# Kernel optimization log

Measured on AMD Instinct MI355X. Metric: run time of the kernel, lower is better.

The kernel has to match this reference:

```python
import jax, jax.numpy as jnp
import numpy as np

N_LAYERS = 6
E_DIM = 128
H_DIM = 768
N_HEADS = 12
D_FFN = 3072
SEQ_L = 512
N_WORD = 30000
BATCH = 4
D_HEAD = H_DIM // N_HEADS


def matrix_r(L, d, reverse=False):
    # sinusoidal position matrix, matching torch matrixR
    inv_freq = 1.0 / (10000.0 ** (np.arange(0, d, 2, dtype=np.float32) / d))
    t = np.outer(np.arange(L, dtype=np.float32), inv_freq)
    mat = np.zeros((L, d), dtype=np.float32)
    mat[:, 0::2] = np.sin(t)
    mat[:, 1::2] = np.cos(t)
    if reverse:
        mat = mat[::-1].copy()
    return jnp.asarray(mat)


def _ln(x, g, b, eps=1e-5):
    mu = jnp.mean(x, axis=-1, keepdims=True)
    var = jnp.mean((x - mu) ** 2, axis=-1, keepdims=True)
    return (x - mu) / jnp.sqrt(var + eps) * g + b


def _gelu(x):
    return x * jax.nn.sigmoid(1.702 * x)


def _shift(B):
    # Transformer-XL shift/skew trick: prepend zero column, reshape, drop row, tril
    b, h, L, _ = B.shape
    z = jnp.zeros((b, h, L, 1), B.dtype)
    return jnp.tril(jnp.concatenate([z, B], axis=-1).reshape(b, h, L + 1, L)[:, :, 1:, :])


def _attn_block(x, R, Wq, Wke, Wv, Wkr, cb, pb, Wo_w, Wo_b, g1, b1):
    b, L, H = x.shape
    h, dh = N_HEADS, D_HEAD
    q = (x @ Wq).reshape(b, L, h, dh).transpose(0, 2, 1, 3)   # bhld
    k = (x @ Wke).reshape(b, L, h, dh).transpose(0, 2, 1, 3)
    v = (x @ Wv).reshape(b, L, h, dh).transpose(0, 2, 1, 3)
    Q = (R @ Wkr).reshape(L, h, dh).transpose(1, 0, 2)        # (h, L, dh)
    A_a = jnp.einsum('bhid,bhjd->bhij', q, k)                  # content-content
    Bt = jnp.einsum('bhid,hjd->bhij', q, Q)                    # content-position
    cb_h = cb.reshape(h, dh)
    pb_h = pb.reshape(h, dh)
    A_c = jnp.einsum('hd,bhjd->bhj', cb_h, k)[:, :, None, :]   # global content bias
    D_row = jnp.einsum('hd,hjd->hj', pb_h, Q)                  # global position bias
    D = jnp.broadcast_to(D_row[None, :, None, :], (b, h, L, L))
    A = A_a + _shift(Bt) + A_c + _shift(D)                     # no 1/sqrt(d) scaling in source
    p = jax.nn.softmax(A, axis=-1)
    Oh = jnp.einsum('bhij,bhjd->bhid', p, v)
    O = Oh.transpose(0, 2, 1, 3).reshape(b, L, H)
    return _ln(x + O @ Wo_w + Wo_b, g1, b1)


def setup_inputs() -> dict:
    key = jax.random.key(0)
    ks = jax.random.split(key, 20)
    s = 0.02

    def nrm(k, shape):
        return jax.random.normal(k, shape, jnp.float32) * s

    N, H, F, L = N_LAYERS, H_DIM, D_FFN, SEQ_L
    R0 = matrix_r(L, H, reverse=True)
    inp = {
        'batch': jax.random.randint(ks[0], (BATCH, SEQ_L), 0, N_WORD),
        'seglens': jax.random.randint(ks[1], (BATCH, 2), 0, 200),
        'tok_emb': nrm(ks[2], (N_WORD, E_DIM)),
        'to_hid_w': nrm(ks[3], (E_DIM, H)),
        'to_hid_b': jnp.zeros((H,), jnp.float32),
        'R': jnp.broadcast_to(R0[None], (N, L, H)).copy() if hasattr(jnp.broadcast_to(R0[None], (N, L, H)), 'copy') else jnp.tile(R0[None], (N, 1, 1)),
        'Wq': nrm(ks[4], (N, H, H)),
        'Wke': nrm(ks[5], (N, H, H)),
        'Wv': nrm(ks[6], (N, H, H)),
        'Wkr': nrm(ks[7], (N, H, H)),
        'cb': jnp.ones((N, H), jnp.float32),
        'pb': jnp.ones((N, H), jnp.float32),
        'Wo_w': nrm(ks[8], (N, H, H)),
        'Wo_b': jnp.zeros((N, H), jnp.float32),
        'ln1_g': jnp.ones((N, H), jnp.float32),
        'ln1_b': jnp.zeros((N, H), jnp.float32),
        'ff1_w': nrm(ks[9], (N, H, F)),
        'ff1_b': jnp.zeros((N, F), jnp.float32),
        'ff2_w': nrm(ks[10], (N, F, H)),
        'ff2_b': jnp.zeros((N, H), jnp.float32),
        'ln2_g': jnp.ones((N, H), jnp.float32),
        'ln2_b': jnp.zeros((N, H), jnp.float32),
        'osp_w': nrm(ks[11], (H, 2)),
        'osp_b': jnp.zeros((2,), jnp.float32),
        'mlm_w': nrm(ks[12], (H, H)),
        'mlm_b': jnp.zeros((H,), jnp.float32),
        'mlm_ln_g': jnp.ones((H,), jnp.float32),
        'mlm_ln_b': jnp.zeros((H,), jnp.float32),
        'to_emb_w': nrm(ks[13], (H, E_DIM)),
        'to_emb_b': jnp.zeros((E_DIM,), jnp.float32),
        'out_b': jnp.zeros((N_WORD,), jnp.float32),
    }
    return inp


def reference(batch, seglens, tok_emb, to_hid_w, to_hid_b, R, Wq, Wke, Wv, Wkr, cb, pb,
              Wo_w, Wo_b, ln1_g, ln1_b, ff1_w, ff1_b, ff2_w, ff2_b, ln2_g, ln2_b,
              osp_w, osp_b, mlm_w, mlm_b, mlm_ln_g, mlm_ln_b, to_emb_w, to_emb_b, out_b):
    # seglens is unused by the original forward (mode='pretrain')
    pe = matrix_r(SEQ_L, H_DIM)[None]                      # (1, L, H) absolute positions
    x = tok_emb[batch] @ to_hid_w + to_hid_b + pe          # (B, L, H)
    for i in range(N_LAYERS):
        x = _attn_block(x, R[i], Wq[i], Wke[i], Wv[i], Wkr[i], cb[i], pb[i],
                        Wo_w[i], Wo_b[i], ln1_g[i], ln1_b[i])
        x = _ln(x + _gelu(x @ ff1_w[i] + ff1_b[i]) @ ff2_w[i] + ff2_b[i], ln2_g[i], ln2_b[i])
    C = x[:, 0, :] @ osp_w + osp_b                          # (B, 2) SOP head
    m = _ln(_gelu(x[:, 1:, :] @ mlm_w + mlm_b), mlm_ln_g, mlm_ln_b)
    T = (m @ to_emb_w + to_emb_b) @ tok_emb.T + out_b       # (B, L-1, n_word) tied logits
    return (C, T)
```

## Files before the change

### kernel.cpp

```cpp
#include <hip/hip_runtime.h>
#include <hip/hip_bf16.h>
#include <math.h>

typedef __hip_bfloat16 bf16;
typedef unsigned short ushort_t;
typedef __attribute__((ext_vector_type(8))) short bf16x8;
typedef __attribute__((ext_vector_type(4))) float f32x4;

#define N_LAYERS 6
#define E_DIM 128
#define H_DIM 768
#define N_HEADS 12
#define D_FFN 3072
#define SEQ_L 512
#define N_WORD 30000
#define BATCH 4
#define D_HEAD 64

__device__ __forceinline__ float ldin(const void* p, long i, int fb) {
    return fb ? __bfloat162float(((const bf16*)p)[i]) : ((const float*)p)[i];
}
__device__ __forceinline__ void stout(void* p, long i, float v, int fb) {
    if (fb) ((bf16*)p)[i] = __float2bfloat16(v);
    else    ((float*)p)[i] = v;
}

__global__ void detect_k(const void* g, int* flag)
{
    if (threadIdx.x == 0) {
        const unsigned short* u = (const unsigned short*)g;
        *flag = (u[0] == 0x3F80u) ? 1 : 0;
    }
}

__global__ __launch_bounds__(256)
void embed_k(const int* __restrict__ batch, const void* __restrict__ emb,
             const void* __restrict__ W, const void* __restrict__ bvec,
             float* __restrict__ x, const int* __restrict__ flagp)
{
    int fb = *flagp;
    int tkn = blockIdx.x;
    int l = tkn & 511;
    int idx = batch[tkn];
    __shared__ float e[E_DIM];
    int t = threadIdx.x;
    if (t < E_DIM) e[t] = ldin(emb, (long)idx * E_DIM + t, fb);
    __syncthreads();
    for (int j = t; j < H_DIM; j += 256) {
        float s = 0.f;
        #pragma unroll 8
        for (int k = 0; k < E_DIM; ++k) s += e[k] * ldin(W, (long)k * H_DIM + j, fb);
        s += ldin(bvec, j, fb);
        int m2 = j & ~1;
        float inv = powf(10000.f, -(float)m2 / 768.f);
        float tt = (float)l * inv;
        s += (j & 1) ? cosf(tt) : sinf(tt);
        x[(long)tkn * H_DIM + j] = s;
    }
}

__device__ __forceinline__ void split8(const float* v, uint4& hi, uint4& lo)
{
    unsigned h[4], l[4];
    #pragma unroll
    for (int u = 0; u < 4; ++u) {
        float a = v[2 * u], b = v[2 * u + 1];
        unsigned ba = __float_as_uint(a), bb = __float_as_uint(b);
        unsigned ha = ba & 0xFFFF0000u, hb = bb & 0xFFFF0000u;
        float la = a - __uint_as_float(ha);
        float lb = b - __uint_as_float(hb);
        h[u] = (ha >> 16) | hb;
        l[u] = (__float_as_uint(la) >> 16) | (__float_as_uint(lb) & 0xFFFF0000u);
    }
    hi = make_uint4(h[0], h[1], h[2], h[3]);
    lo = make_uint4(l[0], l[1], l[2], l[3]);
}

template<int BM, int BN, int TPB>
__global__ __launch_bounds__(TPB)
void gemm2(const void* __restrict__ Ap, long aoff0, int lda, long sA1, long sA2,
           const void* __restrict__ Bp, long boff0, int ldb, long sB1, long sB2,
           float* __restrict__ Cp, long coff0, int ldc, long sC1, long sC2,
           int N, int K, int nb2,
           const void* __restrict__ bias, long biasoff, int bstr, int bfp32, int act,
           int amode, int bmode, int bT, int cmode, int flip, int qkv,
           const void* __restrict__ Bp1, const void* __restrict__ Bp2,
           const void* __restrict__ Bp3,
           const void* __restrict__ ApR, long aoffR, float* __restrict__ CpR,
           long cqstride,
           const int* __restrict__ flagp)
{
    constexpr int WAVES = TPB / 64;
    constexpr int WC = (BN >= 128) ? 4 : 2;
    constexpr int WR = WAVES / WC;
    constexpr int FM = (BM / WR) / 16;
    constexpr int FN = (BN / WC) / 16;
    constexpr int AS = BM * 8;
    constexpr int BS = BN * 8;
    constexpr int APT = AS / TPB;
    constexpr int BPT = BS / TPB;
    static_assert(APT >= 1 && BPT >= 1, "tile/threads");

    __shared__ uint4 sAh[AS], sAl[AS], sBh[BS], sBl[BS];

    int fb = *flagp;
    int z = blockIdx.z;
    int z1 = z / nb2, z2 = z - z1 * nb2;
    int I0 = (flip ? blockIdx.x : blockIdx.y) * BM;
    int J0 = (flip ? blockIdx.y : blockIdx.x) * BN;

    const void* A = Ap;
    const void* B = Bp;
    long aoff = aoff0 + z1 * sA1 + z2 * sA2;
    long bofz = boff0 + z1 * sB1 + z2 * sB2;
    float* C = Cp + coff0 + z1 * sC1 + z2 * sC2;
    int am = amode;

    if (qkv) {
        if (z == 3) {
            if (I0 >= 512) return;
            A = ApR; aoff = aoffR; am = 1; C = CpR;
            B = Bp3;
        } else {
            A = Ap; aoff = aoff0;
            B = (z == 0) ? Bp : (z == 1) ? Bp1 : Bp2;
            C = Cp + coff0 + (long)z * cqstride;
        }
        bofz = boff0;
    }

    bool abf = (am == 1) && fb;
    bool bbf = (bmode == 1) && fb;

    int t = threadIdx.x;
    int lane = t & 63;
    int w = t >> 6, wr = w / WC, wc = w % WC;

    f32x4 acc[FM][FN];
    #pragma unroll
    for (int m = 0; m < FM; ++m)
        #pragma unroll
        for (int n = 0; n < FN; ++n)
            #pragma unroll
            for (int q = 0; q < 4; ++q) acc[m][n][q] = 0.f;

    float fA[APT][8]; uint4 uA[APT];
    float fB[BPT][8]; uint4 uB[BPT];
    ushort_t hBv[BPT][8];

    auto FETCH = [&](int k0) {
        #pragma unroll
        for (int p = 0; p < APT; ++p) {
            int s = t + p * TPB;
            int fi = s >> 6, ln = s & 63;
            int ks = fi / (BM / 16), fr = fi - ks * (BM / 16);
            int r = fr * 16 + (ln & 15);
            int kc = ks * 32 + ((ln >> 4) & 3) * 8;
            long g = aoff + (long)(I0 + r) * lda + (k0 + kc);
            if (abf) {
                uA[p] = *(const uint4*)((const ushort_t*)A + g);
            } else {
                *(float4*)&fA[p][0] = *(const float4*)((const float*)A + g);
                *(float4*)&fA[p][4] = *(const float4*)((const float*)A + g + 4);
            }
        }
        #pragma unroll
        for (int p = 0; p < BPT; ++p) {
            int s = t + p * TPB;
            int fi = s >> 6, ln = s & 63;
            int ks = fi / (BN / 16), fc = fi - ks * (BN / 16);
            int col = fc * 16 + (ln & 15);
            int kc = ks * 32 + ((ln >> 4) & 3) * 8;
            int gc = J0 + col;
            if (bT) {
                bool ok = gc < N;
                long g = bofz + (long)gc * ldb + (k0 + kc);
                if (bbf) {
                    uB[p] = ok ? *(const uint4*)((const ushort_t*)B + g)
                               : make_uint4(0, 0, 0, 0);
                } else if (ok) {
                    *(float4*)&fB[p][0] = *(const float4*)((const float*)B + g);
                    *(float4*)&fB[p][4] = *(const float4*)((const float*)B + g + 4);
                } else {
                    #pragma unroll
                    for (int u = 0; u < 8; ++u) fB[p][u] = 0.f;
                }
            } else {
                long g = bofz + (long)(k0 + kc) * ldb + gc;
                if (bbf) {
                    #pragma unroll
                    for (int u = 0; u < 8; ++u)
                        hBv[p][u] = ((const ushort_t*)B)[g + (long)u * ldb];
                } else {
                    #pragma unroll
                    for (int u = 0; u < 8; ++u)
                        fB[p][u] = ((const float*)B)[g + (long)u * ldb];
                }
            }
        }
    };

    auto STORE = [&]() {
        #pragma unroll
        for (int p = 0; p < APT; ++p) {
            int s = t + p * TPB;
            if (abf) {
                sAh[s] = uA[p];
            } else {
                uint4 hi, lo; split8(fA[p], hi, lo);
                sAh[s] = hi; sAl[s] = lo;
            }
        }
        #pragma unroll
        for (int p = 0; p < BPT; ++p) {
            int s = t + p * TPB;
            if (bbf) {
                if (bT) sBh[s] = uB[p];
                else sBh[s] = make_uint4(
                    (unsigned)hBv[p][0] | ((unsigned)hBv[p][1] << 16),
                    (unsigned)hBv[p][2] | ((unsigned)hBv[p][3] << 16),
                    (unsigned)hBv[p][4] | ((unsigned)hBv[p][5] << 16),
                    (unsigned)hBv[p][6] | ((unsigned)hBv[p][7] << 16));
            } else {
                uint4 hi, lo; split8(fB[p], hi, lo);
                sBh[s] = hi; sBl[s] = lo;
            }
        }
    };

    auto COMPUTE = [&]() {
        #pragma unroll
        for (int ks = 0; ks < 2; ++ks) {
            const bf16x8* Ah = (const bf16x8*)sAh + ks * (BM / 16) * 64;
            const bf16x8* Al = (const bf16x8*)sAl + ks * (BM / 16) * 64;
            const bf16x8* Bh = (const bf16x8*)sBh + ks * (BN / 16) * 64;
            const bf16x8* Bl = (const bf16x8*)sBl + ks * (BN / 16) * 64;
            bf16x8 ah[FM], bh[FN];
            #pragma unroll
            for (int m = 0; m < FM; ++m) ah[m] = Ah[(wr * FM + m) * 64 + lane];
            #pragma unroll
            for (int n = 0; n < FN; ++n) bh[n] = Bh[(wc * FN + n) * 64 + lane];
            #pragma unroll
            for (int m = 0; m < FM; ++m)
                #pragma unroll
                for (int n = 0; n < FN; ++n)
                    acc[m][n] = __builtin_amdgcn_mfma_f32_16x16x32_bf16(
                        ah[m], bh[n], acc[m][n], 0, 0, 0);
            if (!abf) {
                bf16x8 al[FM];
                #pragma unroll
                for (int m = 0; m < FM; ++m) al[m] = Al[(wr * FM + m) * 64 + lane];
                #pragma unroll
                for (int m = 0; m < FM; ++m)
                    #pragma unroll
                    for (int n = 0; n < FN; ++n)
                        acc[m][n] = __builtin_amdgcn_mfma_f32_16x16x32_bf16(
                            al[m], bh[n], acc[m][n], 0, 0, 0);
            }
            if (!bbf) {
                bf16x8 bl[FN];
                #pragma unroll
                for (int n = 0; n < FN; ++n) bl[n] = Bl[(wc * FN + n) * 64 + lane];
                #pragma unroll
                for (int m = 0; m < FM; ++m)
                    #pragma unroll
                    for (int n = 0; n < FN; ++n)
                        acc[m][n] = __builtin_amdgcn_mfma_f32_16x16x32_bf16(
                            ah[m], bl[n], acc[m][n], 0, 0, 0);
            }
        }
    };

    FETCH(0);
    for (int k0 = 0; k0 < K; k0 += 64) {
        STORE();
        __syncthreads();
        if (k0 + 64 < K) FETCH(k0 + 64);
        COMPUTE();
        __syncthreads();
    }

    int rl = (lane >> 4) * 4, cl = lane & 15;
    if (cmode == 0) {
        #pragma unroll
        for (int m = 0; m < FM; ++m) {
            #pragma unroll
            for (int n = 0; n < FN; ++n) {
                int col = J0 + wc * (BN / WC) + n * 16 + cl;
                float bv = 0.f;
                if (bias) bv = bfp32 ? ((const float*)bias)[biasoff + (long)z2 * bstr + col]
                                     : ldin(bias, biasoff + (long)z2 * bstr + col, fb);
                #pragma unroll
                for (int j = 0; j < 4; ++j) {
                    int row = I0 + wr * (BM / WR) + m * 16 + rl + j;
                    float v = acc[m][n][j] + bv;
                    if (act == 1) v = v / (1.f + expf(-1.702f * v));
                    C[(long)row * ldc + col] = v;
                }
            }
        }
    } else {
        #pragma unroll
        for (int m = 0; m < FM; ++m) {
            #pragma unroll
            for (int n = 0; n < FN; ++n) {
                int col = J0 + wc * (BN / WC) + n * 16 + cl;
                if (col >= N) continue;
                float bv = ldin(bias, biasoff + col, fb);
                #pragma unroll
                for (int j = 0; j < 4; ++j) {
                    int row = I0 + wr * (BM / WR) + m * 16 + rl + j;
                    int b = row >> 9, l = row & 511;
                    if (l == 0) continue;
                    long ri = (long)b * 511 + (l - 1);
                    stout((void*)C, 8 + ri * (long)N_WORD + col, acc[m][n][j] + bv, fb);
                }
            }
        }
    }
}

__global__ __launch_bounds__(256)
void attn_k(const float* __restrict__ qb, const float* __restrict__ kb,
            const float* __restrict__ vb, const float* __restrict__ BQ,
            const float* __restrict__ kkb, float* __restrict__ out, int bq0)
{
    __shared__ uint4 sQh[512], sQl[512];
    __shared__ uint4 sKh[512], sKl[512];
    __shared__ uint4 sVh[512], sVl[512];
    __shared__ ushort_t sPh[4096], sPl[4096];

    int qt = blockIdx.x;
    int by = blockIdx.y;
    int h  = by % 12;
    int bq = bq0 + by / 12;
    const float* BQh = BQ + (long)by * 262144;
    const float* kkrow = kkb + ((long)(bq * 12 + h)) * 512;
    long qrow0 = (long)bq * 512 + qt * 64;
    long krow0 = (long)bq * 512;

    int t = threadIdx.x;
    int lane = t & 63;
    int w = t >> 6;
    int l4 = (lane >> 4) & 3, l15 = lane & 15;

    #pragma unroll
    for (int p = 0; p < 2; ++p) {
        int s = t + p * 256;
        int fi = s >> 6, ln = s & 63;
        int ks = fi >> 2, fr = fi & 3;
        int r = fr * 16 + (ln & 15);
        int kc = ks * 32 + ((ln >> 4) & 3) * 8;
        const float* g = qb + (qrow0 + r) * 768 + h * 64 + kc;
        float v[8];
        *(float4*)(v)     = *(const float4*)g;
        *(float4*)(v + 4) = *(const float4*)(g + 4);
        uint4 hi, lo; split8(v, hi, lo);
        sQh[s] = hi; sQl[s] = lo;
    }
    __syncthreads();
    bf16x8 qh[2], ql[2];
    #pragma unroll
    for (int ks = 0; ks < 2; ++ks) {
        qh[ks] = ((const bf16x8*)sQh)[(ks * 4 + w) * 64 + lane];
        ql[ks] = ((const bf16x8*)sQl)[(ks * 4 + w) * 64 + lane];
    }

    float mrun[4], lrun[4];
    f32x4 oacc[4];
    #pragma unroll
    for (int j = 0; j < 4; ++j) { mrun[j] = -3e38f; lrun[j] = 0.f; }
    #pragma unroll
    for (int n = 0; n < 4; ++n)
        #pragma unroll
        for (int j = 0; j < 4; ++j) oacc[n][j] = 0.f;

    for (int kt = 0; kt < 8; ++kt) {
        __syncthreads();
        #pragma unroll
        for (int p = 0; p < 2; ++p) {
            int s = t + p * 256;
            int fi = s >> 6, ln = s & 63;
            int ks = fi >> 2, fc = fi & 3;
            int j = fc * 16 + (ln & 15);
            int kc = ks * 32 + ((ln >> 4) & 3) * 8;
            const float* g = kb + (krow0 + kt * 64 + j) * 768 + h * 64 + kc;
            float v[8];
            *(float4*)(v)     = *(const float4*)g;
            *(float4*)(v + 4) = *(const float4*)(g + 4);
            uint4 hi, lo; split8(v, hi, lo);
            sKh[s] = hi; sKl[s] = lo;
        }
        #pragma unroll
        for (int p = 0; p < 2; ++p) {
            int s = t + p * 256;
            int fi = s >> 6, ln = s & 63;
            int ks = fi >> 2, fd = fi & 3;
            int d = fd * 16 + (ln & 15);
            int j0 = ks * 32 + ((ln >> 4) & 3) * 8;
            float v[8];
            #pragma unroll
            for (int u = 0; u < 8; ++u)
                v[u] = vb[(krow0 + kt * 64 + j0 + u) * 768 + h * 64 + d];
            uint4 hi, lo; split8(v, hi, lo);
            sVh[s] = hi; sVl[s] = lo;
        }
        __syncthreads();

        f32x4 sc[4];
        #pragma unroll
        for (int n = 0; n < 4; ++n)
            #pragma unroll
            for (int j = 0; j < 4; ++j) sc[n][j] = 0.f;
        #pragma unroll
        for (int ks = 0; ks < 2; ++ks) {
            bf16x8 kh[4], kl[4];
            #pragma unroll
            for (int n = 0; n < 4; ++n) {
                kh[n] = ((const bf16x8*)sKh)[(ks * 4 + n) * 64 + lane];
                kl[n] = ((const bf16x8*)sKl)[(ks * 4 + n) * 64 + lane];
// ... 72 lines not shown
            #pragma unroll
            for (int n = 0; n < 4; ++n) {
                oacc[n] = __builtin_amdgcn_mfma_f32_16x16x32_bf16(pa,  vh[n], oacc[n], 0, 0, 0);
                oacc[n] = __builtin_amdgcn_mfma_f32_16x16x32_bf16(pl2, vh[n], oacc[n], 0, 0, 0);
                oacc[n] = __builtin_amdgcn_mfma_f32_16x16x32_bf16(pa,  vl[n], oacc[n], 0, 0, 0);
            }
        }
    }

    #pragma unroll
    for (int n = 0; n < 4; ++n)
        #pragma unroll
        for (int jj = 0; jj < 4; ++jj) {
            int rp = w * 16 + l4 * 4 + jj;
            int cp = n * 16 + l15;
            out[(qrow0 + rp) * 768 + h * 64 + cp] = oacc[n][jj] / lrun[jj];
        }
}

__global__ __launch_bounds__(256)
void kbias_k(const float* __restrict__ kmat, const void* __restrict__ cb,
             long cboff, float* __restrict__ kk, const int* __restrict__ flagp)
{
    int fb = *flagp;
    int idx = blockIdx.x * 256 + threadIdx.x;
    int j = idx & 511;
    int z = idx >> 9;
    int h = z % 12, b = z / 12;
    const float* kr = kmat + ((long)(b * 512 + j)) * H_DIM + h * 64;
    float s = 0.f;
    #pragma unroll 8
    for (int d = 0; d < 64; ++d) s += kr[d] * ldin(cb, cboff + h * 64 + d, fb);
    kk[idx] = s;
}

__global__ __launch_bounds__(256)
void drow_k(const float* __restrict__ Qp, const void* __restrict__ pb,
            long pboff, float* __restrict__ Drow, const int* __restrict__ flagp)
{
    int fb = *flagp;
    int idx = blockIdx.x * 256 + threadIdx.x;
    int j = idx & 511;
    int h = idx >> 9;
    const float* qr = Qp + (long)j * H_DIM + h * 64;
    float s = 0.f;
    #pragma unroll 8
    for (int d = 0; d < 64; ++d) s += qr[d] * ldin(pb, pboff + h * 64 + d, fb);
    Drow[h * 512 + j] = s;
}

__global__ __launch_bounds__(256)
void ln_k(const float* y, const float* resid,
          const void* bias, long biasoff, const void* g, long goff,
          const void* bta, long boff, float* out, const int* flagp)
{
    int fb = *flagp;
    long row = blockIdx.x;
    const float* yr = y + row * H_DIM;
    int t = threadIdx.x;
    float v[3];
    #pragma unroll
    for (int i = 0; i < 3; ++i) {
        int c = t + i * 256;
        float x = yr[c];
        if (resid) x += resid[row * H_DIM + c];
        if (bias) x += ldin(bias, biasoff + c, fb);
        v[i] = x;
    }
    __shared__ float red[256];
    red[t] = v[0] + v[1] + v[2];
    __syncthreads();
    for (int s = 128; s > 0; s >>= 1) { if (t < s) red[t] += red[t + s]; __syncthreads(); }
    float mu = red[0] / 768.f;
    __syncthreads();
    float d0 = v[0] - mu, d1 = v[1] - mu, d2 = v[2] - mu;
    red[t] = d0 * d0 + d1 * d1 + d2 * d2;
    __syncthreads();
    for (int s = 128; s > 0; s >>= 1) { if (t < s) red[t] += red[t + s]; __syncthreads(); }
    float rs = rsqrtf(red[0] / 768.f + 1e-5f);
    float* outr = out + row * H_DIM;
    float dd[3] = {d0, d1, d2};
    #pragma unroll
    for (int i = 0; i < 3; ++i) {
        int c = t + i * 256;
        outr[c] = dd[i] * rs * ldin(g, goff + c, fb) + ldin(bta, boff + c, fb);
    }
}

__global__ __launch_bounds__(256)
void sop_k(const float* __restrict__ x, const void* __restrict__ w,
           const void* __restrict__ bias, void* __restrict__ out,
           const int* __restrict__ flagp)
{
    int fb = *flagp;
    int b = blockIdx.x >> 1, o = blockIdx.x & 1;
    int t = threadIdx.x;
    const float* xr = x + (long)b * 512 * H_DIM;
    float s = 0.f;
    for (int c = t; c < H_DIM; c += 256) s += xr[c] * ldin(w, (long)c * 2 + o, fb);
    __shared__ float red[256];
    red[t] = s;
    __syncthreads();
    for (int st = 128; st > 0; st >>= 1) { if (t < st) red[t] += red[t + st]; __syncthreads(); }
    if (t == 0) stout(out, blockIdx.x, red[0] + ldin(bias, o, fb), fb);
}

extern "C" void kernel_launch(void* const* d_in, const int* in_sizes, int n_in,
                              void* d_out, int out_size, void* d_ws, size_t ws_size,
                              hipStream_t stream)
{
    const int*  batch    = (const int*)d_in[0];
    const void* tok_emb  = d_in[2];
    const void* to_hid_w = d_in[3];
    const void* to_hid_b = d_in[4];
// ... 12 lines not shown
    const void* ff1_b    = d_in[17];
    const void* ff2_w    = d_in[18];
    const void* ff2_b    = d_in[19];
    const void* ln2_g    = d_in[20];
    const void* ln2_b    = d_in[21];
    const void* osp_w    = d_in[22];
    const void* osp_b    = d_in[23];
    const void* mlm_w    = d_in[24];
    const void* mlm_b    = d_in[25];
    const void* mlm_ln_g = d_in[26];
    const void* mlm_ln_b = d_in[27];
    const void* to_emb_w = d_in[28];
    const void* to_emb_b = d_in[29];
    const void* out_b    = d_in[30];

    float* ws  = (float*)d_ws;
    float* x   = ws;
    float* qb  = ws + 1572864;
    float* kb  = ws + 3145728;
    float* vb  = ws + 4718592;
    float* tmp = ws + 6291456;
    float* U   = ws + 7864320;
    float* Qp  = ws + 11010048;
    float* kkb = ws + 11403264;
    float* Dr  = ws + 11427840;
    int*   flg = (int*)(ws + 11433984);
    float* G   = ws + 3145728;
    float* eb  = qb;

    const bool big = ws_size >= (size_t)96200000;
    float* BQb = big ? (ws + 11440000) : U;

    const void* NP = nullptr;
    float* NF = nullptr;

    detect_k<<<1, 64, 0, stream>>>(ln1_g, flg);
    embed_k<<<2048, 256, 0, stream>>>(batch, tok_emb, to_hid_w, to_hid_b, x, flg);

    for (int i = 0; i < N_LAYERS; ++i) {
        long oW  = (long)i * 768 * 768;
        long o768 = (long)i * 768;
        long oR  = (long)i * 512 * 768;
        long oF1 = (long)i * 768 * 3072;
        long oF2 = (long)i * 3072 * 768;

        gemm2<128,128,512><<<dim3(6,16,4), 512, 0, stream>>>(
            x, 0, 768, 0, 0,  Wq, oW, 768, 0, 0,  qb, 0, 768, 0, 0,
            768, 768, 1,  NP, 0, 0, 0, 0,  0, 1, 0, 0, 0, 1,
            Wke, Wv, Wkr,  R, oR, Qp, 1572864, flg);

        kbias_k<<<96, 256, 0, stream>>>(kb, cb, o768, kkb, flg);
        drow_k<<<24, 256, 0, stream>>>(Qp, pb, o768, Dr, flg);

        if (big) {
            gemm2<128,128,512><<<dim3(4,4,48), 512, 0, stream>>>(
                qb, 0, 768, 393216, 64,  Qp, 0, 768, 0, 64,
                BQb, 0, 512, 3145728, 262144,
                512, 64, 12,  Dr, 0, 512, 1, 0,  0, 0, 1, 0, 0, 0,
                NP, NP, NP, NP, 0, NF, 0, flg);
            attn_k<<<dim3(8,48), 256, 0, stream>>>(qb, kb, vb, BQb, kkb, tmp, 0);
        } else {
            for (int bq = 0; bq < BATCH; ++bq) {
                gemm2<128,128,512><<<dim3(4,4,12), 512, 0, stream>>>(
                    qb, (long)bq * 393216, 768, 0, 64,  Qp, 0, 768, 0, 64,
                    U, 0, 512, 0, 262144,
                    512, 64, 12,  Dr, 0, 512, 1, 0,  0, 0, 1, 0, 0, 0,
                    NP, NP, NP, NP, 0, NF, 0, flg);
                attn_k<<<dim3(8,12), 256, 0, stream>>>(qb, kb, vb, U, kkb, tmp, bq);
            }
        }

        gemm2<64,64,256><<<dim3(12,32,1), 256, 0, stream>>>(
            tmp, 0, 768, 0, 0,  Wo_w, oW, 768, 0, 0,  qb, 0, 768, 0, 0,
            768, 768, 1,  NP, 0, 0, 0, 0,  0, 1, 0, 0, 0, 0,
            NP, NP, NP, NP, 0, NF, 0, flg);
        ln_k<<<2048, 256, 0, stream>>>(qb, x, Wo_b, o768, ln1_g, o768, ln1_b, o768, x, flg);

        gemm2<128,128,512><<<dim3(24,16,1), 512, 0, stream>>>(
            x, 0, 768, 0, 0,  ff1_w, oF1, 3072, 0, 0,  G, 0, 3072, 0, 0,
            3072, 768, 1,  ff1_b, (long)i * 3072, 0, 0, 1,  0, 1, 0, 0, 0, 0,
            NP, NP, NP, NP, 0, NF, 0, flg);
        gemm2<64,64,256><<<dim3(12,32,1), 256, 0, stream>>>(
            G, 0, 3072, 0, 0,  ff2_w, oF2, 768, 0, 0,  qb, 0, 768, 0, 0,
            768, 3072, 1,  NP, 0, 0, 0, 0,  0, 1, 0, 0, 0, 0,
            NP, NP, NP, NP, 0, NF, 0, flg);
        ln_k<<<2048, 256, 0, stream>>>(qb, x, ff2_b, o768, ln2_g, o768, ln2_b, o768, x, flg);
    }

    sop_k<<<8, 256, 0, stream>>>(x, osp_w, osp_b, d_out, flg);

    gemm2<64,64,256><<<dim3(12,32,1), 256, 0, stream>>>(
        x, 0, 768, 0, 0,  mlm_w, 0, 768, 0, 0,  tmp, 0, 768, 0, 0,
        768, 768, 1,  mlm_b, 0, 0, 0, 1,  0, 1, 0, 0, 0, 0,
        NP, NP, NP, NP, 0, NF, 0, flg);
    ln_k<<<2048, 256, 0, stream>>>(tmp, nullptr, nullptr, 0, mlm_ln_g, 0, mlm_ln_b, 0, kb, flg);
    gemm2<64,64,256><<<dim3(2,32,1), 256, 0, stream>>>(
        kb, 0, 768, 0, 0,  to_emb_w, 0, 128, 0, 0,  eb, 0, 128, 0, 0,
        128, 768, 1,  to_emb_b, 0, 0, 0, 0,  0, 1, 0, 0, 0, 0,
        NP, NP, NP, NP, 0, NF, 0, flg);
    gemm2<128,128,512><<<dim3(16,235,1), 512, 0, stream>>>(
        eb, 0, 128, 0, 0,  tok_emb, 0, 128, 0, 0,  (float*)d_out, 0, 0, 0, 0,
        30000, 128, 1,  out_b, 0, 0, 0, 0,  0, 1, 1, 1, 1, 0,
        NP, NP, NP, NP, 0, NF, 0, flg);
}
```

Measured before the change: 3.726 ms.

## Store activations as pre-split bf16 hi/lo planes instead of fp32

```diff
diff --git a/kernel.cpp b/kernel.cpp
--- a/kernel.cpp
+++ b/kernel.cpp
@@ -17,12 +17,41 @@
 #define BATCH 4
 #define D_HEAD 64
 
+#define UOFF_X    0L
+#define PLX       1572864L
+#define UOFF_QB   3145728L
+#define UOFF_KB   6291456L
+#define UOFF_VB   9437184L
+#define UOFF_TMP  12582912L
+#define UOFF_G    6291456L
+#define PLG       6291456L
+#define UOFF_QP   22020096L
+#define PLQP      393216L
+#define UOFF_EB   3145728L
+#define PLEB      262144L
+#define FOFF_U    7864320L
+#define FOFF_KKB  11403264L
+#define FOFF_DR   11427840L
+#define FOFF_FLG  11433984L
+#define FOFF_BQ   11440000L
+
 __device__ __forceinline__ float ldin(const void* p, long i, int fb) {
     return fb ? __bfloat162float(((const bf16*)p)[i]) : ((const float*)p)[i];
 }
 __device__ __forceinline__ void stout(void* p, long i, float v, int fb) {
     if (fb) ((bf16*)p)[i] = __float2bfloat16(v);
     else    ((float*)p)[i] = v;
+}
+__device__ __forceinline__ float b2f(ushort_t u) {
+    return __uint_as_float((unsigned)u << 16);
+}
+__device__ __forceinline__ float prd(const ushort_t* h, long pl, long i) {
+    return b2f(h[i]) + b2f(h[pl + i]);
+}
+__device__ __forceinline__ void pwr(ushort_t* h, long pl, long i, float v) {
+    unsigned hb = __float_as_uint(v) & 0xFFFF0000u;
+    h[i] = (ushort_t)(hb >> 16);
+    h[pl + i] = (ushort_t)(__float_as_uint(v - __uint_as_float(hb)) >> 16);
 }
 
 __global__ void detect_k(const void* g, int* flag)
@@ -36,7 +65,7 @@
 __global__ __launch_bounds__(256)
 void embed_k(const int* __restrict__ batch, const void* __restrict__ emb,
              const void* __restrict__ W, const void* __restrict__ bvec,
-             float* __restrict__ x, const int* __restrict__ flagp)
+             ushort_t* __restrict__ x, const int* __restrict__ flagp)
 {
     int fb = *flagp;
     int tkn = blockIdx.x;
@@ -55,7 +84,7 @@
         float inv = powf(10000.f, -(float)m2 / 768.f);
         float tt = (float)l * inv;
         s += (j & 1) ? cosf(tt) : sinf(tt);
-        x[(long)tkn * H_DIM + j] = s;
+        pwr(x, PLX, (long)tkn * H_DIM + j, s);
     }
 }
 
@@ -78,16 +107,16 @@
 
 template<int BM, int BN, int TPB>
 __global__ __launch_bounds__(TPB)
-void gemm2(const void* __restrict__ Ap, long aoff0, int lda, long sA1, long sA2,
-           const void* __restrict__ Bp, long boff0, int ldb, long sB1, long sB2,
-           float* __restrict__ Cp, long coff0, int ldc, long sC1, long sC2,
+void gemm3(const void* __restrict__ Ap, long aoff0, long apl, int lda, long sA1, long sA2, int amode,
+           const void* __restrict__ Bp, long boff0, long bpl, int ldb, long sB1, long sB2, int bmode, int bT,
+           void* __restrict__ Cp, long coff0, long cpl, int ldc, long sC1, long sC2, int cfmt,
            int N, int K, int nb2,
            const void* __restrict__ bias, long biasoff, int bstr, int bfp32, int act,
-           int amode, int bmode, int bT, int cmode, int flip, int qkv,
+           int flip, int qkv,
            const void* __restrict__ Bp1, const void* __restrict__ Bp2,
            const void* __restrict__ Bp3,
-           const void* __restrict__ ApR, long aoffR, float* __restrict__ CpR,
-           long cqstride,
+           const void* __restrict__ ApR, long aoffR, void* __restrict__ CpR,
+           long cplR, long cqstride,
            const int* __restrict__ flagp)
 {
     constexpr int WAVES = TPB / 64;
@@ -101,7 +130,11 @@
     constexpr int BPT = BS / TPB;
     static_assert(APT >= 1 && BPT >= 1, "tile/threads");
 
-    __shared__ uint4 sAh[AS], sAl[AS], sBh[BS], sBl[BS];
+    __shared__ uint4 smem[2 * AS + 2 * BS];
+    uint4* sAh = smem;
+    uint4* sAl = smem + AS;
+    uint4* sBh = smem + 2 * AS;
+    uint4* sBl = smem + 2 * AS + BS;
 
     int fb = *flagp;
     int z = blockIdx.z;
@@ -113,24 +146,31 @@
     const void* B = Bp;
     long aoff = aoff0 + z1 * sA1 + z2 * sA2;
     long bofz = boff0 + z1 * sB1 + z2 * sB2;
-    float* C = Cp + coff0 + z1 * sC1 + z2 * sC2;
     int am = amode;
+    long cplv = cpl;
+    float* Cf = nullptr;
+    ushort_t* Ch = nullptr;
+    if (cfmt == 0) Cf = (float*)Cp + coff0 + z1 * sC1 + z2 * sC2;
+    else if (cfmt == 2) Ch = (ushort_t*)Cp + coff0 + z1 * sC1 + z2 * sC2;
 
     if (qkv) {
         if (z == 3) {
             if (I0 >= 512) return;
-            A = ApR; aoff = aoffR; am = 1; C = CpR;
+            A = ApR; aoff = aoffR; am = 1;
             B = Bp3;
+            Ch = (ushort_t*)CpR; cplv = cplR;
         } else {
             A = Ap; aoff = aoff0;
             B = (z == 0) ? Bp : (z == 1) ? Bp1 : Bp2;
-            C = Cp + coff0 + (long)z * cqstride;
+            Ch = (ushort_t*)Cp + coff0 + (long)z * cqstride;
         }
         bofz = boff0;
     }
 
     bool abf = (am == 1) && fb;
     bool bbf = (bmode == 1) && fb;
+    bool aLo = !abf;
+    bool bLo = !bbf;
 
     int t = threadIdx.x;
     int lane = t & 63;
@@ -144,9 +184,8 @@
             #pragma unroll
             for (int q = 0; q < 4; ++q) acc[m][n][q] = 0.f;
 
-    float fA[APT][8]; uint4 uA[APT];
-    float fB[BPT][8]; uint4 uB[BPT];
-    ushort_t hBv[BPT][8];
+    uint4 uA[APT][2], uB[BPT][2];
+    uint4 z4 = make_uint4(0, 0, 0, 0);
 
     auto FETCH = [&](int k0) {
         #pragma unroll
@@ -157,11 +196,14 @@
             int r = fr * 16 + (ln & 15);
             int kc = ks * 32 + ((ln >> 4) & 3) * 8;
             long g = aoff + (long)(I0 + r) * lda + (k0 + kc);
-            if (abf) {
-                uA[p] = *(const uint4*)((const ushort_t*)A + g);
+            if (am == 0) {
+                uA[p][0] = *(const uint4*)((const ushort_t*)A + g);
+                uA[p][1] = *(const uint4*)((const ushort_t*)A + apl + g);
+            } else if (abf) {
+                uA[p][0] = *(const uint4*)((const ushort_t*)A + g);
             } else {
-                *(float4*)&fA[p][0] = *(const float4*)((const float*)A + g);
-                *(float4*)&fA[p][4] = *(const float4*)((const float*)A + g + 4);
+                *(float4*)&uA[p][0] = *(const float4*)((const float*)A + g);
+                *(float4*)&uA[p][1] = *(const float4*)((const float*)A + g + 4);
             }
         }
         #pragma unroll
@@ -172,29 +214,32 @@
             int col = fc * 16 + (ln & 15);
             int kc = ks * 32 + ((ln >> 4) & 3) * 8;
             int gc = J0 + col;
-            if (bT) {
+            if (bmode == 0) {
+                bool ok = gc < N;
+                long g = bofz + (long)gc * ldb + (k0 + kc);
+                uB[p][0] = ok ? *(const uint4*)((const ushort_t*)B + g) : z4;
+                uB[p][1] = ok ? *(const uint4*)((const ushort_t*)B + bpl + g) : z4;
+            } else if (bT) {
                 bool ok = gc < N;
                 long g = bofz + (long)gc * ldb + (k0 + kc);
                 if (bbf) {
-                    uB[p] = ok ? *(const uint4*)((const ushort_t*)B + g)
-                               : make_uint4(0, 0, 0, 0);
+                    uB[p][0] = ok ? *(const uint4*)((const ushort_t*)B + g) : z4;
                 } else if (ok) {
-                    *(float4*)&fB[p][0] = *(const float4*)((const float*)B + g);
-                    *(float4*)&fB[p][4] = *(const float4*)((const float*)B + g + 4);
-                } else {
-                    #pragma unroll
-                    for (int u = 0; u < 8; ++u) fB[p][u] = 0.f;
-                }
+                    *(float4*)&uB[p][0] = *(const float4*)((const float*)B + g);
+                    *(float4*)&uB[p][1] = *(const float4*)((const float*)B + g + 4);
+                } else { uB[p][0] = z4; uB[p][1] = z4; }
             } else {
                 long g = bofz + (long)(k0 + kc) * ldb + gc;
                 if (bbf) {
+                    ushort_t* hb = (ushort_t*)&uB[p][0];
                     #pragma unroll
                     for (int u = 0; u < 8; ++u)
-                        hBv[p][u] = ((const ushort_t*)B)[g + (long)u * ldb];
+                        hb[u] = ((const ushort_t*)B)[g + (long)u * ldb];
                 } else {
+                    float* fB = (float*)&uB[p][0];
                     #pragma unroll
                     for (int u = 0; u < 8; ++u)
-                        fB[p][u] = ((const float*)B)[g + (long)u * ldb];
+                        fB[u] = ((const float*)B)[g + (long)u * ldb];
                 }
             }
         }
@@ -204,27 +249,16 @@
         #pragma unroll
         for (int p = 0; p < APT; ++p) {
             int s = t + p * TPB;
-            if (abf) {
-                sAh[s] = uA[p];
-            } else {
-                uint4 hi, lo; split8(fA[p], hi, lo);
-                sAh[s] = hi; sAl[s] = lo;
-            }
+            if (am == 0) { sAh[s] = uA[p][0]; sAl[s] = uA[p][1]; }
+            else if (abf) { sAh[s] = uA[p][0]; }
+            else { uint4 hi, lo; split8((const float*)&uA[p][0], hi, lo); sAh[s] = hi; sAl[s] = lo; }
         }
         #pragma unroll
         for (int p = 0; p < BPT; ++p) {
             int s = t + p * TPB;
-            if (bbf) {
-                if (bT) sBh[s] = uB[p];
-                else sBh[s] = make_uint4(
-                    (unsigned)hBv[p][0] | ((unsigned)hBv[p][1] << 16),
-                    (unsigned)hBv[p][2] | ((unsigned)hBv[p][3] << 16),
-                    (unsigned)hBv[p][4] | ((unsigned)hBv[p][5] << 16),
-                    (unsigned)hBv[p][6] | ((unsigned)hBv[p][7] << 16));
-            } else {
-                uint4 hi, lo; split8(fB[p], hi, lo);
-                sBh[s] = hi; sBl[s] = lo;
-            }
+            if (bmode == 0) { sBh[s] = uB[p][0]; sBl[s] = uB[p][1]; }
+            else if (bbf) { sBh[s] = uB[p][0]; }
+            else { uint4 hi, lo; split8((const float*)&uB[p][0], hi, lo); sBh[s] = hi; sBl[s] = lo; }
         }
     };
 
@@ -246,7 +280,7 @@
                 for (int n = 0; n < FN; ++n)
                     acc[m][n] = __builtin_amdgcn_mfma_f32_16x16x32_bf16(
                         ah[m], bh[n], acc[m][n], 0, 0, 0);
-            if (!abf) {
+            if (aLo) {
                 bf16x8 al[FM];
                 #pragma unroll
                 for (int m = 0; m < FM; ++m) al[m] = Al[(wr * FM + m) * 64 + lane];
@@ -257,7 +291,7 @@
                         acc[m][n] = __builtin_amdgcn_mfma_f32_16x16x32_bf16(
                             al[m], bh[n], acc[m][n], 0, 0, 0);
             }
-            if (!bbf) {
+            if (bLo) {
                 bf16x8 bl[FN];
                 #pragma unroll
                 for (int n = 0; n < FN; ++n) bl[n] = Bl[(wc * FN + n) * 64 + lane];
@@ -281,7 +315,64 @@
     }
 
     int rl = (lane >> 4) * 4, cl = lane & 15;
-    if (cmode == 0) {
+    if (cfmt == 1) {
+        float* sC = (float*)smem;
+        #pragma unroll
+        for (int m = 0; m < FM; ++m)
+            #pragma unroll
+            for (int n = 0; n < FN; ++n) {
+                int col = wc * (BN / WC) + n * 16 + cl;
+                #pragma unroll
+                for (int j = 0; j < 4; ++j) {
+                    int row = wr * (BM / WR) + m * 16 + rl + j;
+                    sC[row * BN + col] = acc[m][n][j];
+                }
+            }
+        __syncthreads();
+        for (int tt = t; tt < BM * (BN / 32); tt += TPB) {
+            int r2 = tt / (BN / 32);
+            int c0 = (tt % (BN / 32)) * 32;
+            int grow = I0 + r2;
+            int bI = grow >> 9, li = grow & 511;
+            if (li == 0) continue;
+            int gc0 = J0 + c0;
+            long ro = 8 + ((long)bI * 511 + li - 1) * (long)N_WORD + gc0;
+            if (gc0 + 32 <= N) {
+                if (fb) {
+                    #pragma unroll
+                    for (int q8 = 0; q8 < 4; ++q8) {
+                        unsigned pk[4];
+                        #pragma unroll
+                        for (int c2 = 0; c2 < 4; ++c2) {
+                            float v0 = sC[r2 * BN + c0 + q8 * 8 + c2 * 2] + ldin(bias, biasoff + gc0 + q8 * 8 + c2 * 2, fb);
+                            float v1 = sC[r2 * BN + c0 + q8 * 8 + c2 * 2 + 1] + ldin(bias, biasoff + gc0 + q8 * 8 + c2 * 2 + 1, fb);
+                            bf16 b0 = __float2bfloat16(v0), b1 = __float2bfloat16(v1);
+                            pk[c2] = (unsigned)*reinterpret_cast<ushort_t*>(&b0)
+                                   | ((unsigned)*reinterpret_cast<ushort_t*>(&b1) << 16);
+                        }
+                        *(uint4*)((ushort_t*)Cp + ro + q8 * 8) = make_uint4(pk[0], pk[1], pk[2], pk[3]);
+                    }
+                } else {
+                    #pragma unroll
+                    for (int q4 = 0; q4 < 8; ++q4) {
+                        float4 fv;
+                        fv.x = sC[r2 * BN + c0 + q4 * 4 + 0] + ldin(bias, biasoff + gc0 + q4 * 4 + 0, fb);
+                        fv.y = sC[r2 * BN + c0 + q4 * 4 + 1] + ldin(bias, biasoff + gc0 + q4 * 4 + 1, fb);
+                        fv.z = sC[r2 * BN + c0 + q4 * 4 + 2] + ldin(bias, biasoff + gc0 + q4 * 4 + 2, fb);
+                        fv.w = sC[r2 * BN + c0 + q4 * 4 + 3] + ldin(bias, biasoff + gc0 + q4 * 4 + 3, fb);
+                        *(float4*)((float*)Cp + ro + q4 * 4) = fv;
+                    }
+                }
+            } else {
+                for (int c = 0; c < 32; ++c) {
+                    int gc = gc0 + c;
+                    if (gc >= N) break;
+                    float v = sC[r2 * BN + c0 + c] + ldin(bias, biasoff + gc, fb);
+                    stout(Cp, ro + c, v, fb);
+                }
+            }
+        }
+    } else {
         #pragma unroll
         for (int m = 0; m < FM; ++m) {
             #pragma unroll
@@ -294,41 +385,33 @@
                 for (int j = 0; j < 4; ++j) {
                     int row = I0 + wr * (BM / WR) + m * 16 + rl + j;
                     float v = acc[m][n][j] + bv;
-                    if (act == 1) v = v / (1.f + expf(-1.702f * v));
-                    C[(long)row * ldc + col] = v;
+                    if (act == 1) v = v / (1.f + __expf(-1.702f * v));
+                    long ci = (long)row * ldc + col;
+                    if (cfmt == 0) Cf[ci] = v;
+                    else {
+                        unsigned hb = __float_as_uint(v) & 0xFFFF0000u;
+                        Ch[ci] = (ushort_t)(hb >> 16);
+                        Ch[cplv + ci] = (ushort_t)(__float_as_uint(v - __uint_as_float(hb)) >> 16);
+                    }
                 }
             }
         }
-    } else {
-        #pragma unroll
-        for (int m = 0; m < FM; ++m) {
-            #pragma unroll
-            for (int n = 0; n < FN; ++n) {
-                int col = J0 + wc * (BN / WC) + n * 16 + cl;
-                if (col >= N) continue;
-                float bv = ldin(bias, biasoff + col, fb);
-                #pragma unroll
-                for (int j = 0; j < 4; ++j) {
-                    int row = I0 + wr * (BM / WR) + m * 16 + rl + j;
-                    int b = row >> 9, l = row & 511;
-                    if (l == 0) continue;
-                    long ri = (long)b * 511 + (l - 1);
-                    stout((void*)C, 8 + ri * (long)N_WORD + col, acc[m][n][j] + bv, fb);
-                }
-            }
-        }
     }
 }
 
 __global__ __launch_bounds__(256)
-void attn_k(const float* __restrict__ qb, const float* __restrict__ kb,
-            const float* __restrict__ vb, const float* __restrict__ BQ,
-            const float* __restrict__ kkb, float* __restrict__ out, int bq0)
+void attn_k(ushort_t* __restrict__ uws, const float* __restrict__ BQ,
+            const float* __restrict__ kkb, int bq0)
 {
     __shared__ uint4 sQh[512], sQl[512];
     __shared__ uint4 sKh[512], sKl[512];
     __shared__ uint4 sVh[512], sVl[512];
     __shared__ ushort_t sPh[4096], sPl[4096];
+
+    const ushort_t* qbh = uws + UOFF_QB;
+    const ushort_t* kbh = uws + UOFF_KB;
+    const ushort_t* vbh = uws + UOFF_VB;
+    ushort_t* outp = uws + UOFF_TMP;
 
     int qt = blockIdx.x;
     int by = blockIdx.y;
@@ -351,12 +434,9 @@
         int ks = fi >> 2, fr = fi & 3;
         int r = fr * 16 + (ln & 15);
         int kc = ks * 32 + ((ln >> 4) & 3) * 8;
-        const float* g = qb + (qrow0 + r) * 768 + h * 64 + kc;
-        float v[8];
-        *(float4*)(v)     = *(const float4*)g;
-        *(float4*)(v + 4) = *(const float4*)(g + 4);
-        uint4 hi, lo; split8(v, hi, lo);
-        sQh[s] = hi; sQl[s] = lo;
+        long g = (qrow0 + r) * 768 + h * 64 + kc;
+        sQh[s] = *(const uint4*)(qbh + g);
+        sQl[s] = *(const uint4*)(qbh + PLX + g);
     }
     __syncthreads();
     bf16x8 qh[2], ql[2];
@@ -384,12 +464,9 @@
             int ks = fi >> 2, fc = fi & 3;
             int j = fc * 16 + (ln & 15);
             int kc = ks * 32 + ((ln >> 4) & 3) * 8;
-            const float* g = kb + (krow0 + kt * 64 + j) * 768 + h * 64 + kc;
-            float v[8];
-            *(float4*)(v)     = *(const float4*)g;
-            *(float4*)(v + 4) = *(const float4*)(g + 4);
-            uint4 hi, lo; split8(v, hi, lo);
-            sKh[s] = hi; sKl[s] = lo;
+            long g = (krow0 + kt * 64 + j) * 768 + h * 64 + kc;
+            sKh[s] = *(const uint4*)(kbh + g);
+            sKl[s] = *(const uint4*)(kbh + PLX + g);
         }
         #pragma unroll
         for (int p = 0; p < 2; ++p) {
@@ -398,12 +475,16 @@
             int ks = fi >> 2, fd = fi & 3;
             int d = fd * 16 + (ln & 15);
             int j0 = ks * 32 + ((ln >> 4) & 3) * 8;
-            float v[8];
-            #pragma unroll
-            for (int u = 0; u < 8; ++u)
-                v[u] = vb[(krow0 + kt * 64 + j0 + u) * 768 + h * 64 + d];
-            uint4 hi, lo; split8(v, hi, lo);
-            sVh[s] = hi; sVl[s] = lo;
+            uint4 hv, lv;
+            ushort_t* hp = (ushort_t*)&hv;
+            ushort_t* lp = (ushort_t*)&lv;
+            #pragma unroll
+            for (int u = 0; u < 8; ++u) {
+                long gi = (krow0 + kt * 64 + j0 + u) * 768 + h * 64 + d;
+                hp[u] = vbh[gi];
+                lp[u] = vbh[PLX + gi];
+            }
+            sVh[s] = hv; sVl[s] = lv;
         }
         __syncthreads();
 
@@ -506,56 +587,55 @@
         for (int jj = 0; jj < 4; ++jj) {
             int rp = w * 16 + l4 * 4 + jj;
             int cp = n * 16 + l15;
-            out[(qrow0 + rp) * 768 + h * 64 + cp] = oacc[n][jj] / lrun[jj];
+            pwr(outp, PLX, (qrow0 + rp) * 768 + h * 64 + cp, oacc[n][jj] / lrun[jj]);
         }
 }
 
 __global__ __launch_bounds__(256)
-void kbias_k(const float* __restrict__ kmat, const void* __restrict__ cb,
-             long cboff, float* __restrict__ kk, const int* __restrict__ flagp)
+void bias_k(const ushort_t* __restrict__ uws, const void* __restrict__ cb,
+            long cboff, const void* __restrict__ pb, long pboff,
+            float* __restrict__ kkb, float* __restrict__ Dr,
+            const int* __restrict__ flagp)
 {
     int fb = *flagp;
-    int idx = blockIdx.x * 256 + threadIdx.x;
-    int j = idx & 511;
-    int z = idx >> 9;
-    int h = z % 12, b = z / 12;
-    const float* kr = kmat + ((long)(b * 512 + j)) * H_DIM + h * 64;
-    float s = 0.f;
-    #pragma unroll 8
-    for (int d = 0; d < 64; ++d) s += kr[d] * ldin(cb, cboff + h * 64 + d, fb);
-    kk[idx] = s;
+    int gb = blockIdx.x, t = threadIdx.x;
+    if (gb < 96) {
+        int idx = gb * 256 + t;
+        int j = idx & 511, z = idx >> 9;
+        int h = z % 12, b = z / 12;
+        const ushort_t* kr = uws + UOFF_KB + ((long)(b * 512 + j)) * 768 + h * 64;
+        float s = 0.f;
+        #pragma unroll 8
+        for (int d = 0; d < 64; ++d)
+            s += (b2f(kr[d]) + b2f(kr[PLX + d])) * ldin(cb, cboff + h * 64 + d, fb);
+        kkb[idx] = s;
+    } else {
+        int idx = (gb - 96) * 256 + t;
+        int j = idx & 511, h = idx >> 9;
+        const ushort_t* qr = uws + UOFF_QP + (long)j * 768 + h * 64;
+        float s = 0.f;
+        #pragma unroll 8
+        for (int d = 0; d < 64; ++d)
+            s += (b2f(qr[d]) + b2f(qr[PLQP + d])) * ldin(pb, pboff + h * 64 + d, fb);
+        Dr[h * 512 + j] = s;
+    }
 }
 
 __global__ __launch_bounds__(256)
-void drow_k(const float* __restrict__ Qp, const void* __restrict__ pb,
-            long pboff, float* __restrict__ Drow, const int* __restrict__ flagp)
-{
-    int fb = *flagp;
-    int idx = blockIdx.x * 256 + threadIdx.x;
-    int j = idx & 511;
-    int h = idx >> 9;
-    const float* qr = Qp + (long)j * H_DIM + h * 64;
-    float s = 0.f;
-    #pragma unroll 8
-    for (int d = 0; d < 64; ++d) s += qr[d] * ldin(pb, pboff + h * 64 + d, fb);
-    Drow[h * 512 + j] = s;
-}
-
-__global__ __launch_bounds__(256)
-void ln_k(const float* y, const float* resid,
+void ln_k(const ushort_t* y, const ushort_t* resid,
           const void* bias, long biasoff, const void* g, long goff,
-          const void* bta, long boff, float* out, const int* flagp)
+          const void* bta, long boff, ushort_t* out, const int* flagp)
 {
     int fb = *flagp;
     long row = blockIdx.x;
-    const float* yr = y + row * H_DIM;
     int t = threadIdx.x;
     float v[3];
     #pragma unroll
     for (int i = 0; i < 3; ++i) {
         int c = t + i * 256;
-        float x = yr[c];
-        if (resid) x += resid[row * H_DIM + c];
+        long idx = row * H_DIM + c;
+        float x = b2f(y[idx]) + b2f(y[PLX + idx]);
+        if (resid) x += b2f(resid[idx]) + b2f(resid[PLX + idx]);
         if (bias) x += ldin(bias, biasoff + c, fb);
         v[i] = x;
     }
@@ -570,26 +650,27 @@
     __syncthreads();
     for (int s = 128; s > 0; s >>= 1) { if (t < s) red[t] += red[t + s]; __syncthreads(); }
     float rs = rsqrtf(red[0] / 768.f + 1e-5f);
-    float* outr = out + row * H_DIM;
     float dd[3] = {d0, d1, d2};
     #pragma unroll
     for (int i = 0; i < 3; ++i) {
         int c = t + i * 256;
-        outr[c] = dd[i] * rs * ldin(g, goff + c, fb) + ldin(bta, boff + c, fb);
+        pwr(out, PLX, row * H_DIM + c, dd[i] * rs * ldin(g, goff + c, fb) + ldin(bta, boff + c, fb));
     }
 }
 
 __global__ __launch_bounds__(256)
-void sop_k(const float* __restrict__ x, const void* __restrict__ w,
+void sop_k(const ushort_t* __restrict__ x, const void* __restrict__ w,
            const void* __restrict__ bias, void* __restrict__ out,
            const int* __restrict__ flagp)
 {
     int fb = *flagp;
     int b = blockIdx.x >> 1, o = blockIdx.x & 1;
     int t = threadIdx.x;
-    const float* xr = x + (long)b * 512 * H_DIM;
     float s = 0.f;
-    for (int c = t; c < H_DIM; c += 256) s += xr[c] * ldin(w, (long)c * 2 + o, fb);
+    for (int c = t; c < H_DIM; c += 256) {
+        long idx = (long)b * 512 * H_DIM + c;
+        s += (b2f(x[idx]) + b2f(x[PLX + idx])) * ldin(w, (long)c * 2 + o, fb);
+    }
     __shared__ float red[256];
     red[t] = s;
     __syncthreads();
@@ -632,28 +713,21 @@
     const void* to_emb_b = d_in[29];
     const void* out_b    = d_in[30];
 
-    float* ws  = (float*)d_ws;
-    float* x   = ws;
-    float* qb  = ws + 1572864;
-    float* kb  = ws + 3145728;
-    float* vb  = ws + 4718592;
-    float* tmp = ws + 6291456;
-    float* U   = ws + 7864320;
-    float* Qp  = ws + 11010048;
-    float* kkb = ws + 11403264;
-    float* Dr  = ws + 11427840;
-    int*   flg = (int*)(ws + 11433984);
-    float* G   = ws + 3145728;
-    float* eb  = qb;
+    float* ws = (float*)d_ws;
+    ushort_t* uws = (ushort_t*)d_ws;
+    float* U   = ws + FOFF_U;
+    float* kkb = ws + FOFF_KKB;
+    float* Dr  = ws + FOFF_DR;
+    int*   flg = (int*)(ws + FOFF_FLG);
+    float* BQf = ws + FOFF_BQ;
 
     const bool big = ws_size >= (size_t)96200000;
-    float* BQb = big ? (ws + 11440000) : U;
 
     const void* NP = nullptr;
-    float* NF = nullptr;
+    void* NF = nullptr;
 
     detect_k<<<1, 64, 0, stream>>>(ln1_g, flg);
-    embed_k<<<2048, 256, 0, stream>>>(batch, tok_emb, to_hid_w, to_hid_b, x, flg);
+    embed_k<<<2048, 256, 0, stream>>>(batch, tok_emb, to_hid_w, to_hid_b, uws, flg);
 
     for (int i = 0; i < N_LAYERS; ++i) {
         long oW  = (long)i * 768 * 768;
@@ -662,62 +736,91 @@
         long oF1 = (long)i * 768 * 3072;
         long oF2 = (long)i * 3072 * 768;
 
-        gemm2<128,128,512><<<dim3(6,16,4), 512, 0, stream>>>(
-            x, 0, 768, 0, 0,  Wq, oW, 768, 0, 0,  qb, 0, 768, 0, 0,
-            768, 768, 1,  NP, 0, 0, 0, 0,  0, 1, 0, 0, 0, 1,
-            Wke, Wv, Wkr,  R, oR, Qp, 1572864, flg);
-
-        kbias_k<<<96, 256, 0, stream>>>(kb, cb, o768, kkb, flg);
-        drow_k<<<24, 256, 0, stream>>>(Qp, pb, o768, Dr, flg);
+        gemm3<128,128,512><<<dim3(6,16,4), 512, 0, stream>>>(
+            uws, UOFF_X, PLX, 768, 0, 0, 0,
+            Wq, oW, 0, 768, 0, 0, 1, 0,
+            uws, UOFF_QB, PLX, 768, 0, 0, 2,
+            768, 768, 1,
+            NP, 0, 0, 0, 0,
+            0, 1,
+            Wke, Wv, Wkr, R, oR, (void*)(uws + UOFF_QP), PLQP, 3145728L,
+            flg);
+
+        bias_k<<<120, 256, 0, stream>>>(uws, cb, o768, pb, o768, kkb, Dr, flg);
 
         if (big) {
-            gemm2<128,128,512><<<dim3(4,4,48), 512, 0, stream>>>(
-                qb, 0, 768, 393216, 64,  Qp, 0, 768, 0, 64,
-                BQb, 0, 512, 3145728, 262144,
-                512, 64, 12,  Dr, 0, 512, 1, 0,  0, 0, 1, 0, 0, 0,
-                NP, NP, NP, NP, 0, NF, 0, flg);
-            attn_k<<<dim3(8,48), 256, 0, stream>>>(qb, kb, vb, BQb, kkb, tmp, 0);
+            gemm3<128,128,512><<<dim3(4,4,48), 512, 0, stream>>>(
+                uws, UOFF_QB, PLX, 768, 393216, 64, 0,
+                uws, UOFF_QP, PLQP, 768, 0, 64, 0, 1,
+                BQf, 0, 0, 512, 3145728, 262144, 0,
+                512, 64, 12,
+                Dr, 0, 512, 1, 0,
+                0, 0, NP, NP, NP, NP, 0, NF, 0, 0, flg);
+            attn_k<<<dim3(8,48), 256, 0, stream>>>(uws, BQf, kkb, 0);
         } else {
             for (int bq = 0; bq < BATCH; ++bq) {
-                gemm2<128,128,512><<<dim3(4,4,12), 512, 0, stream>>>(
-                    qb, (long)bq * 393216, 768, 0, 64,  Qp, 0, 768, 0, 64,
-                    U, 0, 512, 0, 262144,
-                    512, 64, 12,  Dr, 0, 512, 1, 0,  0, 0, 1, 0, 0, 0,
-                    NP, NP, NP, NP, 0, NF, 0, flg);
-                attn_k<<<dim3(8,12), 256, 0, stream>>>(qb, kb, vb, U, kkb, tmp, bq);
-            }
-        }
-
-        gemm2<64,64,256><<<dim3(12,32,1), 256, 0, stream>>>(
-            tmp, 0, 768, 0, 0,  Wo_w, oW, 768, 0, 0,  qb, 0, 768, 0, 0,
-            768, 768, 1,  NP, 0, 0, 0, 0,  0, 1, 0, 0, 0, 0,
-            NP, NP, NP, NP, 0, NF, 0, flg);
-        ln_k<<<2048, 256, 0, stream>>>(qb, x, Wo_b, o768, ln1_g, o768, ln1_b, o768, x, flg);
-
-        gemm2<128,128,512><<<dim3(24,16,1), 512, 0, stream>>>(
-            x, 0, 768, 0, 0,  ff1_w, oF1, 3072, 0, 0,  G, 0, 3072, 0, 0,
-            3072, 768, 1,  ff1_b, (long)i * 3072, 0, 0, 1,  0, 1, 0, 0, 0, 0,
-            NP, NP, NP, NP, 0, NF, 0, flg);
-        gemm2<64,64,256><<<dim3(12,32,1), 256, 0, stream>>>(
-            G, 0, 3072, 0, 0,  ff2_w, oF2, 768, 0, 0,  qb, 0, 768, 0, 0,
-            768, 3072, 1,  NP, 0, 0, 0, 0,  0, 1, 0, 0, 0, 0,
-            NP, NP, NP, NP, 0, NF, 0, flg);
-        ln_k<<<2048, 256, 0, stream>>>(qb, x, ff2_b, o768, ln2_g, o768, ln2_b, o768, x, flg);
-    }
-
-    sop_k<<<8, 256, 0, stream>>>(x, osp_w, osp_b, d_out, flg);
-
-    gemm2<64,64,256><<<dim3(12,32,1), 256, 0, stream>>>(
-        x, 0, 768, 0, 0,  mlm_w, 0, 768, 0, 0,  tmp, 0, 768, 0, 0,
-        768, 768, 1,  mlm_b, 0, 0, 0, 1,  0, 1, 0, 0, 0, 0,
-        NP, NP, NP, NP, 0, NF, 0, flg);
-    ln_k<<<2048, 256, 0, stream>>>(tmp, nullptr, nullptr, 0, mlm_ln_g, 0, mlm_ln_b, 0, kb, flg);
-    gemm2<64,64,256><<<dim3(2,32,1), 256, 0, stream>>>(
-        kb, 0, 768, 0, 0,  to_emb_w, 0, 128, 0, 0,  eb, 0, 128, 0, 0,
-        128, 768, 1,  to_emb_b, 0, 0, 0, 0,  0, 1, 0, 0, 0, 0,
-        NP, NP, NP, NP, 0, NF, 0, flg);
-    gemm2<128,128,512><<<dim3(16,235,1), 512, 0, stream>>>(
-        eb, 0, 128, 0, 0,  tok_emb, 0, 128, 0, 0,  (float*)d_out, 0, 0, 0, 0,
-        30000, 128, 1,  out_b, 0, 0, 0, 0,  0, 1, 1, 1, 1, 0,
-        NP, NP, NP, NP, 0, NF, 0, flg);
-}
+                gemm3<128,128,512><<<dim3(4,4,12), 512, 0, stream>>>(
+                    uws, UOFF_QB + (long)bq * 393216, PLX, 768, 0, 64, 0,
+                    uws, UOFF_QP, PLQP, 768, 0, 64, 0, 1,
+                    U, 0, 0, 512, 0, 262144, 0,
+                    512, 64, 12,
+                    Dr, 0, 512, 1, 0,
+                    0, 0, NP, NP, NP, NP, 0, NF, 0, 0, flg);
+                attn_k<<<dim3(8,12), 256, 0, stream>>>(uws, U, kkb, bq);
+            }
+        }
+
+        gemm3<64,64,256><<<dim3(12,32,1), 256, 0, stream>>>(
+            uws, UOFF_TMP, PLX, 768, 0, 0, 0,
+            Wo_w, oW, 0, 768, 0, 0, 1, 0,
+            uws, UOFF_QB, PLX, 768, 0, 0, 2,
+            768, 768, 1,
+            NP, 0, 0, 0, 0,
+            0, 0, NP, NP, NP, NP, 0, NF, 0, 0, flg);
+        ln_k<<<2048, 256, 0, stream>>>(uws + UOFF_QB, uws, Wo_b, o768,
+                                       ln1_g, o768, ln1_b, o768, uws, flg);
+
+        gemm3<128,128,512><<<dim3(24,16,1), 512, 0, stream>>>(
+            uws, UOFF_X, PLX, 768, 0, 0, 0,
+            ff1_w, oF1, 0, 3072, 0, 0, 1, 0,
+            uws, UOFF_G, PLG, 3072, 0, 0, 2,
+            3072, 768, 1,
+            ff1_b, (long)i * 3072, 0, 0, 1,
+            0, 0, NP, NP, NP, NP, 0, NF, 0, 0, flg);
+        gemm3<64,64,256><<<dim3(12,32,1), 256, 0, stream>>>(
+            uws, UOFF_G, PLG, 3072, 0, 0, 0,
+            ff2_w, oF2, 0, 768, 0, 0, 1, 0,
+            uws, UOFF_QB, PLX, 768, 0, 0, 2,
+            768, 3072, 1,
+            NP, 0, 0, 0, 0,
+            0, 0, NP, NP, NP, NP, 0, NF, 0, 0, flg);
+        ln_k<<<2048, 256, 0, stream>>>(uws + UOFF_QB, uws, ff2_b, o768,
+                                       ln2_g, o768, ln2_b, o768, uws, flg);
+    }
+
+    sop_k<<<8, 256, 0, stream>>>(uws, osp_w, osp_b, d_out, flg);
+
+    gemm3<64,64,256><<<dim3(12,32,1), 256, 0, stream>>>(
+        uws, UOFF_X, PLX, 768, 0, 0, 0,
+        mlm_w, 0, 0, 768, 0, 0, 1, 0,
+        uws, UOFF_TMP, PLX, 768, 0, 0, 2,
+        768, 768, 1,
+        mlm_b, 0, 0, 0, 1,
+        0, 0, NP, NP, NP, NP, 0, NF, 0, 0, flg);
+    ln_k<<<2048, 256, 0, stream>>>(uws + UOFF_TMP, nullptr, nullptr, 0,
+                                   mlm_ln_g, 0, mlm_ln_b, 0, uws + UOFF_KB, flg);
+    gemm3<64,64,256><<<dim3(2,32,1), 256, 0, stream>>>(
+        uws, UOFF_KB, PLX, 768, 0, 0, 0,
+        to_emb_w, 0, 0, 128, 0, 0, 1, 0,
+        uws, UOFF_EB, PLEB, 128, 0, 0, 2,
+        128, 768, 1,
+        to_emb_b, 0, 0, 0, 0,
+        0, 0, NP, NP, NP, NP, 0, NF, 0, 0, flg);
+    gemm3<128,128,512><<<dim3(16,235,1), 512, 0, stream>>>(
+        uws, UOFF_EB, PLEB, 128, 0, 0, 0,
+        tok_emb, 0, 0, 128, 0, 0, 1, 1,
+        d_out, 0, 0, 0, 0, 0, 1,
+        30000, 128, 1,
+        out_b, 0, 0, 0, 0,
+        1, 0, NP, NP, NP, NP, 0, NF, 0, 0, flg);
+}
```

After: 3.838 ms. 1.03x slower.
